# Performance work log

Hardware: AMD Instinct MI355X
Metric: run time of the kernel (lower is better)

Reference implementation:

```python
import jax, jax.numpy as jnp
import numpy as np

N_TOKEN = 267735
CUTOFFS = [20000, 40000, 200000, 267735]
ENDS = [0] + CUTOFFS
CLUSTER_DIMS = [1024, 256, 64, 16]   # d_embed // div_val**i
CLUSTER_SIZES = [20000, 20000, 160000, 67735]
D_PROJ = 1024
T, B = 256, 4
N_CLUSTERS = 3


def setup_inputs() -> dict:
    key = jax.random.key(0)
    ks = jax.random.split(key, 16)
    inp = {}
    inp["hidden"] = jax.random.normal(ks[0], (T, B, D_PROJ), jnp.float32)
    inp["target"] = jax.random.randint(ks[1], (T, B), 0, N_TOKEN)
    for i in range(4):
        inp[f"W{i}"] = jax.random.normal(ks[2 + 3 * i], (CLUSTER_SIZES[i], CLUSTER_DIMS[i]), jnp.float32) * 0.02
        inp[f"b{i}"] = jnp.zeros((CLUSTER_SIZES[i],), jnp.float32)
        inp[f"P{i}"] = jax.random.normal(ks[3 + 3 * i], (CLUSTER_DIMS[i], D_PROJ), jnp.float32) * 0.02
    inp["cluster_weight"] = jax.random.normal(ks[14], (N_CLUSTERS, 1024), jnp.float32) * 0.02
    inp["cluster_bias"] = jnp.zeros((N_CLUSTERS,), jnp.float32)
    return inp


def _logit(x, W, b, P):
    # x: [T,B,d_proj], P: [e,d_proj], W: [n,e] -> [T,B,n]
    y = jnp.einsum('ibd,ed->ibe', x, P)
    return jnp.einsum('ibe,ne->ibn', y, W) + b


def _gather(logprob, tgt):
    # pick logprob[t, b, tgt[t,b]]
    return jnp.take_along_axis(logprob, tgt[..., None], axis=-1)[..., 0]


def reference(hidden, target, W0, b0, P0, W1, b1, P1, W2, b2, P2, W3, b3, P3,
              cluster_weight, cluster_bias):
    Ws = [W0, W1, W2, W3]
    bs = [b0, b1, b2, b3]
    Ps = [P0, P1, P2, P3]
    loss = jnp.zeros(target.shape, jnp.float32)
    head_logprob = None
    for i in range(4):
        l_idx, r_idx = ENDS[i], ENDS[i + 1]
        mask = (target >= l_idx) & (target < r_idx)
        cur_t = jnp.maximum(jnp.minimum(target, r_idx - 1) - l_idx, 0)
        if i == 0:
            Wh = jnp.concatenate([W0, cluster_weight], axis=0)
            bh = jnp.concatenate([b0, cluster_bias], axis=0)
            head_logprob = jax.nn.log_softmax(_logit(hidden, Wh, bh, P0), axis=-1)
            cur_loss = _gather(head_logprob, cur_t)
        else:
            tail_logprob = jax.nn.log_softmax(_logit(hidden, Ws[i], bs[i], Ps[i]), axis=-1)
            logprob_i = head_logprob[..., CUTOFFS[0] + i - 1, None] + tail_logprob
            cur_loss = _gather(logprob_i, cur_t)
        loss = jnp.where(mask, cur_loss, loss)
    return jnp.mean(-loss)
```

## Files before the change

### kernel.cpp

```cpp
#include <hip/hip_runtime.h>
#include <math.h>

typedef short short8 __attribute__((ext_vector_type(8)));
typedef float f32x4 __attribute__((ext_vector_type(4)));
typedef unsigned long long u64;

#define LOG2E 1.4426950408889634f

#if __has_builtin(__builtin_amdgcn_exp2f)
#define EXP2(x) __builtin_amdgcn_exp2f(x)
#else
#define EXP2(x) exp2f(x)
#endif

__device__ __forceinline__ unsigned short f2bf_rne(float f) {
    unsigned u = __float_as_uint(f);
    unsigned r = (u + 0x7fff + ((u >> 16) & 1)) >> 16;
    return (unsigned short)r;
}
__device__ __forceinline__ float bf2f(unsigned short h) {
    return __uint_as_float(((unsigned)h) << 16);
}
__device__ __forceinline__ void load_lds16(const void* g, void* l) {
    __builtin_amdgcn_global_load_lds((const __attribute__((address_space(1))) void*)g,
                                     (__attribute__((address_space(3))) void*)l,
                                     16, 0, 0);
}
template<int N>
__device__ __forceinline__ void waitvm() {
    asm volatile("s_waitcnt vmcnt(%0)" :: "n"(N) : "memory");
}
__device__ __forceinline__ u64 pack8_fp8(const float* v, float s) {
    int lo = 0, hi = 0;
    lo = __builtin_amdgcn_cvt_pk_fp8_f32(v[0] * s, v[1] * s, lo, false);
    lo = __builtin_amdgcn_cvt_pk_fp8_f32(v[2] * s, v[3] * s, lo, true);
    hi = __builtin_amdgcn_cvt_pk_fp8_f32(v[4] * s, v[5] * s, hi, false);
    hi = __builtin_amdgcn_cvt_pk_fp8_f32(v[6] * s, v[7] * s, hi, true);
    return (u64)(unsigned)lo | ((u64)(unsigned)hi << 32);
}

__global__ void cvt_h(const float* __restrict__ in, unsigned short* __restrict__ out)
{
    const int i = blockIdx.x * 256 + threadIdx.x;
    const float4 v = *(const float4*)(in + (size_t)i * 4);
    ushort4 h;
    h.x = f2bf_rne(v.x); h.y = f2bf_rne(v.y);
    h.z = f2bf_rne(v.z); h.w = f2bf_rne(v.w);
    *(ushort4*)(out + (size_t)i * 4) = h;
}

struct ProjDesc {
    const float* B;
    unsigned short* Cbf;
    unsigned char* Cf8;
    int ldc; int nreal; int N; int Kpad; int gy_begin;
};

__global__ __launch_bounds__(256) void prepproj(
    const unsigned short* __restrict__ A,
    ProjDesc p0, ProjDesc p1, ProjDesc p2, ProjDesc p3,
    const float* __restrict__ W0, const float* __restrict__ cw,
    const float* __restrict__ W1, const float* __restrict__ W2,
    const float* __restrict__ W3,
    const float* __restrict__ b0, const float* __restrict__ cb,
    const float* __restrict__ b1, const float* __restrict__ b2,
    const float* __restrict__ b3,
    unsigned char* __restrict__ Wb0, unsigned char* __restrict__ Wb1,
    unsigned char* __restrict__ Wb2, unsigned char* __restrict__ Wb3,
    float* __restrict__ bp)
{
    __shared__ char smem[34816];

    const int tid = threadIdx.x;
    const int bx = blockIdx.x;

    if (bx >= 96) {
        u64* lds = (u64*)smem;
        const int NP = 2596;
        const int nconv = gridDim.x - 96;
        for (int pn = bx - 96; pn < NP; pn += nconv) {
            __syncthreads();
            if (pn < 788) {
                const bool isW0 = (pn < 628);
                const int tile = isW0 ? (pn >> 2) : (pn - 628);
                const int c0 = isW0 ? (pn & 3) * 256 : 0;
                unsigned char* dstm = isW0 ? Wb0 : Wb1;
                const int tstride = isW0 ? 131072 : 32768;
#pragma unroll
                for (int rp = 0; rp < 8; ++rp) {
                    const int row = rp * 16 + (tid >> 4);
                    const int colf = (tid & 15) * 16;
                    const int row_g = tile * 128 + row;
                    const float* s = nullptr;
                    if (isW0) {
                        if (row_g < 20000)      s = W0 + (size_t)row_g * 1024 + c0 + colf;
                        else if (row_g < 20003) s = cw + (size_t)(row_g - 20000) * 1024 + c0 + colf;
                    } else {
                        if (row_g < 20000)      s = W1 + (size_t)row_g * 256 + colf;
                    }
                    float f[16];
                    if (s) {
#pragma unroll
                        for (int q = 0; q < 4; ++q) {
                            const float4 v = *(const float4*)(s + q * 4);
                            f[q * 4 + 0] = v.x; f[q * 4 + 1] = v.y;
                            f[q * 4 + 2] = v.z; f[q * 4 + 3] = v.w;
                        }
                    } else {
#pragma unroll
                        for (int q = 0; q < 16; ++q) f[q] = 0.f;
                    }
                    const int kg = (tid & 15) * 2;
                    lds[kg * 130 + row]       = pack8_fp8(f,     16.0f);
                    lds[(kg + 1) * 130 + row] = pack8_fp8(f + 8, 16.0f);
                }
                __syncthreads();
                u64* dst = (u64*)(dstm + (size_t)tile * tstride) + (size_t)(c0 >> 3) * 128;
#pragma unroll
                for (int i = 0; i < 16; ++i) {
                    const int lin = i * 256 + tid;
                    const int kg = lin >> 7, r = lin & 127;
                    dst[lin] = lds[kg * 130 + r];
                }
            } else if (pn < 2052) {
                const int tile = pn - 788;
#pragma unroll
                for (int rp = 0; rp < 2; ++rp) {
                    const int row = rp * 64 + (tid >> 2);
                    const int colf = (tid & 3) * 16;
                    const int row_g = tile * 128 + row;
                    const float* s = (row_g < 160000) ? W2 + (size_t)row_g * 64 + colf : nullptr;
                    float f[16];
                    if (s) {
#pragma unroll
                        for (int q = 0; q < 4; ++q) {
                            const float4 v = *(const float4*)(s + q * 4);
                            f[q * 4 + 0] = v.x; f[q * 4 + 1] = v.y;
                            f[q * 4 + 2] = v.z; f[q * 4 + 3] = v.w;
                        }
                    } else {
#pragma unroll
                        for (int q = 0; q < 16; ++q) f[q] = 0.f;
                    }
                    const int kg = (tid & 3) * 2;
                    lds[kg * 130 + row]       = pack8_fp8(f,     16.0f);
                    lds[(kg + 1) * 130 + row] = pack8_fp8(f + 8, 16.0f);
                }
                __syncthreads();
                u64* dst = (u64*)(Wb2 + (size_t)tile * 8192);
#pragma unroll
                for (int i = 0; i < 4; ++i) {
                    const int lin = i * 256 + tid;
                    const int kg = lin >> 7, r = lin & 127;
                    dst[lin] = lds[kg * 130 + r];
                }
            } else {
                const int tile = pn - 2052;
                if (tid < 128) {
                    const int row = tid;
                    const int row_g = tile * 128 + row;
                    const float* s = (row_g < 67735) ? W3 + (size_t)row_g * 16 : nullptr;
                    float f[16];
                    if (s) {
#pragma unroll
                        for (int q = 0; q < 4; ++q) {
                            const float4 v = *(const float4*)(s + q * 4);
                            f[q * 4 + 0] = v.x; f[q * 4 + 1] = v.y;
                            f[q * 4 + 2] = v.z; f[q * 4 + 3] = v.w;
                        }
                    } else {
#pragma unroll
                        for (int q = 0; q < 16; ++q) f[q] = 0.f;
                    }
                    lds[row]       = pack8_fp8(f,     16.0f);
                    lds[130 + row] = pack8_fp8(f + 8, 16.0f);
                }
                __syncthreads();
                u64* dst = (u64*)(Wb3 + (size_t)tile * 8192);
#pragma unroll
                for (int i = 0; i < 4; ++i) {
                    const int lin = i * 256 + tid;
                    const int kg = lin >> 7, r = lin & 127;
                    dst[lin] = (kg < 2) ? lds[kg * 130 + r] : 0ull;
                }
            }
        }

        const unsigned BN = 68000u;
        const unsigned stride = (gridDim.x - 96) * 256u;
        for (unsigned u = (bx - 96) * 256u + tid; u < BN; u += stride) {
            const unsigned idx0 = u * 4u;
            float e[4];
#pragma unroll
            for (int j = 0; j < 4; ++j) {
                const unsigned idx = idx0 + j;
                float v;
                if (idx < 20096u) {
                    v = (idx < 20000u) ? b0[idx] * LOG2E
                      : (idx < 20003u) ? cb[idx - 20000u] * LOG2E : -1e30f;
                } else if (idx < 40576u) {
                    const unsigned i1 = idx - 20096u;
                    v = (i1 < 20000u) ? b1[i1] * LOG2E : -1e30f;
                } else if (idx < 202368u) {
                    const unsigned i2 = idx - 40576u;
                    v = (i2 < 160000u) ? b2[i2] * LOG2E : -1e30f;
                } else {
                    const unsigned i3 = idx - 202368u;
                    v = (i3 < 67735u) ? b3[i3] * LOG2E : -1e30f;
                }
                e[j] = v;
            }
            *(float4*)(bp + idx0) = make_float4(e[0], e[1], e[2], e[3]);
        }
        return;
    }

    unsigned short* As = (unsigned short*)smem;
    unsigned short* Bs = (unsigned short*)(smem + 16384);

    const int mt = bx & 7;
    const int py = bx >> 3;
    ProjDesc p = (py >= p3.gy_begin) ? p3 : (py >= p2.gy_begin) ? p2
               : (py >= p1.gy_begin) ? p1 : p0;

    const int w = tid >> 6;
    const int l = tid & 63;
    const int m0 = mt * 128;
    const int n0 = (py - p.gy_begin) * 128;
    const int wm = (w >> 1) * 64;
    const int wn = (w & 1) * 64;
    const int lane16 = l & 15;
    const int quad = l >> 4;

    const unsigned short* aptr[4];
    int ag_base[4];
#pragma unroll
    for (int i = 0; i < 4; ++i) {
        const int g = w * 256 + i * 64 + l;
        aptr[i] = A + (size_t)(m0 + (g & 127)) * 1024 + (g >> 7) * 8;
        ag_base[i] = (w * 256 + i * 64) * 8;
    }

    const int bn = tid >> 1;
    const int bhalf = tid & 1;
    int brow = n0 + bn;
    if (brow > p.N - 1) brow = p.N - 1;
    const float* brow_ptr = p.B + (size_t)brow * 1024;

    f32x4 acc[4][4] = {};

    for (int k0 = 0; k0 < 1024; k0 += 64) {
        __syncthreads();
#pragma unroll
        for (int i = 0; i < 4; ++i)
            load_lds16(aptr[i] + k0, (void*)&As[ag_base[i]]);
#pragma unroll
        for (int j = 0; j < 8; ++j) {
            const int kq = bhalf * 8 + j;
            const float4 v = *(const float4*)(brow_ptr + k0 + kq * 4);
            const unsigned px = __builtin_amdgcn_perm(__float_as_uint(v.y), __float_as_uint(v.x), 0x07060302);
            const unsigned pyv = __builtin_amdgcn_perm(__float_as_uint(v.w), __float_as_uint(v.z), 0x07060302);
            const int gran = (kq >> 1) * 128 + bn;
            *(uint2*)&Bs[gran * 8 + (kq & 1) * 4] = make_uint2(px, pyv);
        }
        __syncthreads();

#pragma unroll
        for (int kk = 0; kk < 2; ++kk) {
            const int kgb = kk * 4 + quad;
            short8 af[4], bfr[4];
#pragma unroll
            for (int mi = 0; mi < 4; ++mi)
                af[mi] = *(const short8*)&As[(kgb * 128 + wm + mi * 16 + lane16) * 8];
#pragma unroll
            for (int ni = 0; ni < 4; ++ni)
                bfr[ni] = *(const short8*)&Bs[(kgb * 128 + wn + ni * 16 + lane16) * 8];
#pragma unroll
            for (int mi = 0; mi < 4; ++mi)
#pragma unroll
                for (int ni = 0; ni < 4; ++ni)
                    acc[mi][ni] = __builtin_amdgcn_mfma_f32_16x16x32_bf16(
                        af[mi], bfr[ni], acc[mi][ni], 0, 0, 0);
        }
    }

#pragma unroll
    for (int mi = 0; mi < 4; ++mi)
#pragma unroll
        for (int ni = 0; ni < 4; ++ni) {
            const int n = n0 + wn + ni * 16 + lane16;
            if (n < p.ldc) {
#pragma unroll
                for (int r = 0; r < 4; ++r) {
                    const int m = m0 + wm + mi * 16 + quad * 4 + r;
                    const float v = (n < p.nreal) ? acc[mi][ni][r] : 0.f;
                    p.Cbf[(size_t)m * p.ldc + n] = f2bf_rne(v);
                }
            }
        }

    float* bounce = (float*)smem;
    u64* Yout = (u64*)p.Cf8 + (size_t)mt * 16 * p.Kpad;
    for (int c = 0; c < 2; ++c) {
        const int colbase = n0 + c * 64;
        if (colbase >= p.Kpad) break;
        __syncthreads();
        if ((w & 1) == c) {
#pragma unroll
            for (int mi = 0; mi < 4; ++mi)
#pragma unroll
                for (int ni = 0; ni < 4; ++ni) {
                    const int ncol = ni * 16 + lane16;
                    const bool real = (colbase + ncol) < p.nreal;
#pragma unroll
                    for (int r = 0; r < 4; ++r) {
                        const int m = wm + mi * 16 + quad * 4 + r;
                        bounce[m * 66 + ncol] = real ? acc[mi][ni][r] : 0.f;
                    }
                }
        }
        __syncthreads();
#pragma unroll
        for (int i = 0; i < 4; ++i) {
            const int g = i * 256 + tid;
            const int kgl = g >> 7;
            const int m = g & 127;
            float v[8];
#pragma unroll
            for (int j = 0; j < 8; ++j) v[j] = bounce[m * 66 + kgl * 8 + j];
            Yout[((colbase >> 3) + kgl) * 128 + m] = pack8_fp8(v, 4.0f);
        }
    }
}

struct ExpDesc {
    const unsigned char* A;
    const unsigned char* W;
    const float* bias;
    float* part;
    int Kpad; int ksl; int kmask; int gy_begin; int slab;
};

__global__ __launch_bounds__(512) void exp_gemm(ExpDesc d0, ExpDesc d1, ExpDesc d2, ExpDesc d3)
{
    __shared__ u64 As[3][2048];
    __shared__ u64 Bs[3][1024];
    __shared__ float biasLds[3][128];

    const int p = blockIdx.x;
    const int gy = blockIdx.y;

    ExpDesc d = (gy >= d3.gy_begin) ? d3 : (gy >= d2.gy_begin) ? d2
              : (gy >= d1.gy_begin) ? d1 : d0;

    const int tid = threadIdx.x;
    const int w = tid >> 6;
    const int l = tid & 63;
    const int wmt = w >> 2;
    const int wq = w & 3;
    const int wm = (wq >> 1) * 64;
    const int wn = (wq & 1) * 64;
    const int lane16 = l & 15;
    const int quad = l >> 4;

    const int tiles_begin = (gy - d.gy_begin) * d.slab;
    const int T = d.slab << d.ksl;
    const int kmask = d.kmask;
    const int ksl = d.ksl;
    const bool haveA = (kmask != 0);

    const size_t tstride = (size_t)128 * d.Kpad;
    const unsigned char* Abase0 = d.A + (size_t)p * tstride;
    const unsigned char* Abase1 = d.A + (size_t)(p + 4) * tstride;
    const unsigned char* Bbase = d.W + (size_t)tiles_begin * tstride;
    const float* biasBase = d.bias + (size_t)tiles_begin * 128;

    const int so = tid * 16;
    const int bu = (w * 4 + l) * 16;

    if (haveA) {
        load_lds16(Abase0 + so, (char*)As[0] + so);
        load_lds16(Abase1 + so, (char*)As[0] + 8192 + so);
        load_lds16(Bbase + so, (char*)Bs[0] + so);
        if (l < 4) load_lds16(biasBase + (bu >> 2), (char*)biasLds + bu);
        load_lds16(Abase0 + 8192 + so, (char*)As[1] + so);
        load_lds16(Abase1 + 8192 + so, (char*)As[1] + 8192 + so);
        load_lds16(Bbase + 8192 + so, (char*)Bs[1] + so);
        if (l < 4) load_lds16(biasBase + (bu >> 2), (char*)biasLds + 512 + bu);
    } else {
        load_lds16(Abase0 + so, (char*)As[0] + so);
        load_lds16(Abase1 + so, (char*)As[0] + 8192 + so);
        load_lds16(Bbase + so, (char*)Bs[0] + so);
        if (l < 4) load_lds16(biasBase + (bu >> 2), (char*)biasLds + bu);
        load_lds16(Bbase + tstride + so, (char*)Bs[1] + so);
        if (l < 4) load_lds16(biasBase + 128 + (bu >> 2), (char*)biasLds + 512 + bu);
    }

    f32x4 acc[4][4] = {};
    float rowsum[4][4] = {};
    const float c1 = LOG2E / 64.0f;

    int slot = 0;
    int ns = 2;
    for (int it = 0; it < T; ++it) {
        if (it + 1 < T) { if (haveA) waitvm<4>(); else waitvm<2>(); }
        else            { waitvm<0>(); }
        __builtin_amdgcn_s_barrier();
        __builtin_amdgcn_sched_barrier(0);

        if (it + 2 < T) {
            const int nit = it + 2;
            const int kc = nit & kmask;
            const int tile = nit >> ksl;
            if (haveA) {
                load_lds16(Abase0 + kc * 8192 + so, (char*)As[ns] + so);
                load_lds16(Abase1 + kc * 8192 + so, (char*)As[ns] + 8192 + so);
            }
            load_lds16(Bbase + (size_t)tile * tstride + kc * 8192 + so, (char*)Bs[ns] + so);
            if (l < 4)
                load_lds16(biasBase + (size_t)tile * 128 + (bu >> 2),
                           (char*)biasLds + ns * 512 + bu);
        }

        const u64* Ar = (haveA ? As[slot] : As[0]) + wmt * 1024;
        const u64* Br = Bs[slot];
#pragma unroll
        for (int ks = 0; ks < 2; ++ks) {
            u64 af[4], bfr[4];
#pragma unroll
            for (int mi = 0; mi < 4; ++mi)
                af[mi] = Ar[(ks * 4 + quad) * 128 + wm + mi * 16 + lane16];
#pragma unroll
            for (int ni = 0; ni < 4; ++ni)
                bfr[ni] = Br[(ks * 4 + quad) * 128 + wn + ni * 16 + lane16];
#pragma unroll
            for (int mi = 0; mi < 4; ++mi)
#pragma unroll
                for (int ni = 0; ni < 4; ++ni)
                    acc[mi][ni] = __builtin_amdgcn_mfma_f32_16x16x32_fp8_fp8(
                        (long)af[mi], (long)bfr[ni], acc[mi][ni], 0, 0, 0);
        }

        if ((it & kmask) == kmask) {
            float biasc[4];
#pragma unroll
            for (int ni = 0; ni < 4; ++ni)
                biasc[ni] = biasLds[slot][wn + ni * 16 + lane16];
#pragma unroll
            for (int mi = 0; mi < 4; ++mi)
#pragma unroll
                for (int r = 0; r < 4; ++r) {
                    float s = EXP2(fmaf(acc[mi][0][r], c1, biasc[0]))
                            + EXP2(fmaf(acc[mi][1][r], c1, biasc[1]))
                            + EXP2(fmaf(acc[mi][2][r], c1, biasc[2]))
                            + EXP2(fmaf(acc[mi][3][r], c1, biasc[3]));
                    rowsum[mi][r] += s;
                }
#pragma unroll
            for (int mi = 0; mi < 4; ++mi)
#pragma unroll
                for (int ni = 0; ni < 4; ++ni)
                    acc[mi][ni] = (f32x4){0.f, 0.f, 0.f, 0.f};
        }

        slot = (slot == 2) ? 0 : slot + 1;
        ns   = (ns   == 2) ? 0 : ns   + 1;
    }

#pragma unroll
    for (int off = 1; off < 16; off <<= 1)
#pragma unroll
        for (int mi = 0; mi < 4; ++mi)
#pragma unroll
            for (int r = 0; r < 4; ++r)
                rowsum[mi][r] += __shfl_xor(rowsum[mi][r], off, 64);

    __syncthreads();
    float* buf = (float*)As;
    if (lane16 == 0) {
#pragma unroll
        for (int mi = 0; mi < 4; ++mi)
#pragma unroll
            for (int r = 0; r < 4; ++r)
                buf[(wmt * 128 + wm + mi * 16 + quad * 4 + r) * 2 + (wn >> 6)] = rowsum[mi][r];
    }
    __syncthreads();
    if (tid < 256) {
        const int row = tid & 127;
        const int mtreal = p + (tid >> 7) * 4;
        d.part[(size_t)(gy - d.gy_begin) * 1024 + mtreal * 128 + row] =
            buf[tid * 2 + 0] + buf[tid * 2 + 1];
    }
}

__global__ void redext(const float* __restrict__ p0, const float* __restrict__ p1,
                       const float* __restrict__ p2, const float* __restrict__ p3,
                       float* __restrict__ S,
                       const unsigned short* __restrict__ Y0, const unsigned short* __restrict__ Y1,
                       const unsigned short* __restrict__ Y2, const unsigned short* __restrict__ Y3,
                       const int* __restrict__ target,
                       const float* __restrict__ W0, const float* __restrict__ b0,
                       const float* __restrict__ W1, const float* __restrict__ b1,
                       const float* __restrict__ W2, const float* __restrict__ b2,
                       const float* __restrict__ W3, const float* __restrict__ b3,
                       const float* __restrict__ cw, const float* __restrict__ cb,
                       float* __restrict__ headlogit, float* __restrict__ taillogit)
{
    if (blockIdx.x < 16) {
        const int idx = blockIdx.x * 256 + threadIdx.x;
        const int c = idx >> 10, m = idx & 1023;
        const float* p = (c == 0) ? p0 : (c == 1) ? p1 : (c == 2) ? p2 : p3;
        const int G = (c == 0) ? 157 : (c == 1) ? 40 : (c == 2) ? 79 : 34;
        float s = 0.f;
        for (int y = 0; y < G; ++y) s += p[(size_t)y * 1024 + m];
        S[idx] = s;
        return;
    }
    const int token = (blockIdx.x - 16) * 4 + (threadIdx.x >> 6);
    const int lane = threadIdx.x & 63;
    const int tgt = target[token];
    const int ci = (tgt < 20000) ? 0 : (tgt < 40000) ? 1 : (tgt < 200000) ? 2 : 3;

    {
        const int h = (ci == 0) ? tgt : (20000 + ci - 1);
        const float* row;
        float bb;
        if (h < 20000) { row = W0 + (size_t)h * 1024; bb = b0[h]; }
        else           { row = cw + (size_t)(h - 20000) * 1024; bb = cb[h - 20000]; }
        const unsigned short* y = Y0 + (size_t)token * 1024;
        float s = 0.f;
        for (int k = lane; k < 1024; k += 64) s += bf2f(y[k]) * row[k];
#pragma unroll
        for (int off = 1; off < 64; off <<= 1) s += __shfl_xor(s, off, 64);
        if (lane == 0) headlogit[token] = s + bb;
    }

    float tl = 0.f;
    if (ci > 0) {
        const unsigned short* Y; const float* W; const float* b; int K, ldy, lidx;
        if (ci == 1)      { Y = Y1; W = W1; b = b1; K = 256; ldy = 256; lidx = 20000; }
        else if (ci == 2) { Y = Y2; W = W2; b = b2; K = 64;  ldy = 64;  lidx = 40000; }
        else              { Y = Y3; W = W3; b = b3; K = 16;  ldy = 64;  lidx = 200000; }
        const int r = tgt - lidx;
        const unsigned short* y = Y + (size_t)token * ldy;
        const float* row = W + (size_t)r * K;
        float s = 0.f;
        for (int k = lane; k < K; k += 64) s += bf2f(y[k]) * row[k];
#pragma unroll
        for (int off = 1; off < 64; off <<= 1) s += __shfl_xor(s, off, 64);
        tl = s + b[r];
    }
    if (lane == 0) taillogit[token] = tl;
}

__global__ void finalize_kernel(const float* __restrict__ S,
                                const int* __restrict__ target,
                                const float* __restrict__ headlogit,
                                const float* __restrict__ taillogit,
                                float* __restrict__ out)
{
    __shared__ float red[256];
    const int tid = threadIdx.x;
    float acc = 0.f;
    for (int token = tid; token < 1024; token += 256) {
        const int tgt = target[token];
        const int ci = (tgt < 20000) ? 0 : (tgt < 40000) ? 1 : (tgt < 200000) ? 2 : 3;
        float lp = headlogit[token] - logf(S[token]);
        if (ci > 0)
            lp += taillogit[token] - logf(S[ci * 1024 + token]);
        acc -= lp;
    }
    red[tid] = acc;
    __syncthreads();
    for (int s = 128; s > 0; s >>= 1) {
        if (tid < s) red[tid] += red[tid + s];
        __syncthreads();
    }
    if (tid == 0) out[0] = red[0] * (1.0f / 1024.0f);
}

extern "C" void kernel_launch(void* const* d_in, const int* in_sizes, int n_in,
                              void* d_out, int out_size, void* d_ws, size_t ws_size,
                              hipStream_t stream)
{
    const float* hidden = (const float*)d_in[0];
    const int*   target = (const int*)d_in[1];
    const float* W0 = (const float*)d_in[2];  const float* b0 = (const float*)d_in[3];  const float* P0 = (const float*)d_in[4];
    const float* W1 = (const float*)d_in[5];  const float* b1 = (const float*)d_in[6];  const float* P1 = (const float*)d_in[7];
    const float* W2 = (const float*)d_in[8];  const float* b2 = (const float*)d_in[9];  const float* P2 = (const float*)d_in[10];
    const float* W3 = (const float*)d_in[11]; const float* b3 = (const float*)d_in[12]; const float* P3 = (const float*)d_in[13];
    const float* cw = (const float*)d_in[14]; const float* cb = (const float*)d_in[15];
    float* out = (float*)d_out;

    unsigned char* ws = (unsigned char*)d_ws;
    unsigned short* h_bf = (unsigned short*)ws;
    unsigned short* Y0bf = (unsigned short*)(ws + 2097152);
    unsigned short* Y1bf = (unsigned short*)(ws + 4194304);
    unsigned short* Y2bf = (unsigned short*)(ws + 4718592);
    unsigned short* Y3bf = (unsigned short*)(ws + 4849664);
    unsigned char* Y0f8 = ws + 4980736;
    unsigned char* Y1f8 = ws + 6029312;
    unsigned char* Y2f8 = ws + 6291456;
    unsigned char* Y3f8 = ws + 6356992;
    unsigned char* Wb0 = ws + 6422528;
    unsigned char* Wb1 = ws + 27000832;
    unsigned char* Wb2 = ws + 32243712;
    unsigned char* Wb3 = ws + 42598400;
    float* bp = (float*)(ws + 47054848);

    float* part0 = (float*)ws;
    float* part1 = part0 + (size_t)157 * 1024;
    float* part2 = part1 + (size_t)40 * 1024;
    float* part3 = part2 + (size_t)79 * 1024;
    float* S = part3 + (size_t)34 * 1024;
    float* headlogit = S + 4096;
    float* taillogit = headlogit + 1024;

    cvt_h<<<1024, 256, 0, stream>>>(hidden, h_bf);

    ProjDesc pr0 = { P0, Y0bf, Y0f8, 1024, 1024, 1024, 1024, 0 };
    ProjDesc pr1 = { P1, Y1bf, Y1f8, 256,  256,  256,  256,  8 };
    ProjDesc pr2 = { P2, Y2bf, Y2f8, 64,   64,   64,   64,   10 };
    ProjDesc pr3 = { P3, Y3bf, Y3f8, 64,   16,   16,   64,   11 };
    prepproj<<<2048, 256, 0, stream>>>(h_bf, pr0, pr1, pr2, pr3,
                                       W0, cw, W1, W2, W3,
                                       b0, cb, b1, b2, b3,
                                       Wb0, Wb1, Wb2, Wb3, bp);

    ExpDesc d0 = { Y0f8, Wb0, bp,          part0, 1024, 4, 15, 0,   1 };
    ExpDesc d1 = { Y1f8, Wb1, bp + 20096,  part1, 256,  2, 3,  157, 4 };
    ExpDesc d2 = { Y2f8, Wb2, bp + 40576,  part2, 64,   0, 0,  197, 16 };
    ExpDesc d3 = { Y3f8, Wb3, bp + 202368, part3, 64,   0, 0,  276, 16 };
    exp_gemm<<<dim3(4, 310), 512, 0, stream>>>(d0, d1, d2, d3);

    redext<<<272, 256, 0, stream>>>(part0, part1, part2, part3, S,
                                    Y0bf, Y1bf, Y2bf, Y3bf, target,
                                    W0, b0, W1, b1, W2, b2, W3, b3,
                                    cw, cb, headlogit, taillogit);

    finalize_kernel<<<1, 256, 0, stream>>>(S, target, headlogit, taillogit, out);
}
```

Before: 353.6 us.

## Double M-tiles per exp_gemm block to reuse W tiles across 1024 threads

Each exp_gemm block now covers four 128-row tiles of activations instead of two, running 1024 threads and half as many blocks along x. Each loaded W/bias tile is reused by twice as many rows, halving global weight traffic. In exchange, LDS per block grows, occupancy may drop, and only half the lanes issue B loads.

Result: slower. 383.0 us (+8.3%).

```diff
diff --git a/kernel.cpp b/kernel.cpp
--- a/kernel.cpp
+++ b/kernel.cpp
@@ -341,9 +341,9 @@
     int Kpad; int ksl; int kmask; int gy_begin; int slab;
 };
 
-__global__ __launch_bounds__(512) void exp_gemm(ExpDesc d0, ExpDesc d1, ExpDesc d2, ExpDesc d3)
+__global__ __launch_bounds__(1024) void exp_gemm(ExpDesc d0, ExpDesc d1, ExpDesc d2, ExpDesc d3)
 {
-    __shared__ u64 As[3][2048];
+    __shared__ u64 As[3][4096];
     __shared__ u64 Bs[3][1024];
     __shared__ float biasLds[3][128];
 
@@ -370,30 +370,36 @@
     const bool haveA = (kmask != 0);
 
     const size_t tstride = (size_t)128 * d.Kpad;
-    const unsigned char* Abase0 = d.A + (size_t)p * tstride;
-    const unsigned char* Abase1 = d.A + (size_t)(p + 4) * tstride;
+    const unsigned char* Abase0 = d.A + (size_t)(p * 4 + 0) * tstride;
+    const unsigned char* Abase1 = d.A + (size_t)(p * 4 + 1) * tstride;
+    const unsigned char* Abase2 = d.A + (size_t)(p * 4 + 2) * tstride;
+    const unsigned char* Abase3 = d.A + (size_t)(p * 4 + 3) * tstride;
     const unsigned char* Bbase = d.W + (size_t)tiles_begin * tstride;
     const float* biasBase = d.bias + (size_t)tiles_begin * 128;
 
     const int so = tid * 16;
-    const int bu = (w * 4 + l) * 16;
-
-    if (haveA) {
-        load_lds16(Abase0 + so, (char*)As[0] + so);
-        load_lds16(Abase1 + so, (char*)As[0] + 8192 + so);
-        load_lds16(Bbase + so, (char*)Bs[0] + so);
-        if (l < 4) load_lds16(biasBase + (bu >> 2), (char*)biasLds + bu);
-        load_lds16(Abase0 + 8192 + so, (char*)As[1] + so);
-        load_lds16(Abase1 + 8192 + so, (char*)As[1] + 8192 + so);
-        load_lds16(Bbase + 8192 + so, (char*)Bs[1] + so);
-        if (l < 4) load_lds16(biasBase + (bu >> 2), (char*)biasLds + 512 + bu);
-    } else {
-        load_lds16(Abase0 + so, (char*)As[0] + so);
-        load_lds16(Abase1 + so, (char*)As[0] + 8192 + so);
-        load_lds16(Bbase + so, (char*)Bs[0] + so);
-        if (l < 4) load_lds16(biasBase + (bu >> 2), (char*)biasLds + bu);
-        load_lds16(Bbase + tstride + so, (char*)Bs[1] + so);
-        if (l < 4) load_lds16(biasBase + 128 + (bu >> 2), (char*)biasLds + 512 + bu);
+    const unsigned char* Asrc01 = (tid < 512) ? Abase0 + so : Abase1 + (so - 8192);
+    const unsigned char* Asrc23 = (tid < 512) ? Abase2 + so : Abase3 + (so - 8192);
+    const int bo = w * 512 + l * 16;
+    const int go = w * 32 + l * 16;
+
+#pragma unroll
+    for (int pit = 0; pit < 2; ++pit) {
+        const int kc = pit & kmask;
+        const int tile = pit >> ksl;
+        if (haveA) {
+            load_lds16(Asrc01 + kc * 8192, (char*)As[pit] + so);
+            load_lds16(Asrc23 + kc * 8192, (char*)As[pit] + 16384 + so);
+        } else if (pit == 0) {
+            load_lds16(Asrc01, (char*)As[0] + so);
+            load_lds16(Asrc23, (char*)As[0] + 16384 + so);
+        }
+        if (l < 32)
+            load_lds16(Bbase + (size_t)tile * tstride + kc * 8192 + bo,
+                       (char*)Bs[pit] + bo);
+        if (l < 2)
+            load_lds16(biasBase + (size_t)tile * 128 + (go >> 2),
+                       (char*)biasLds + pit * 512 + go);
     }
 
     f32x4 acc[4][4] = {};
@@ -413,13 +419,15 @@
             const int kc = nit & kmask;
             const int tile = nit >> ksl;
             if (haveA) {
-                load_lds16(Abase0 + kc * 8192 + so, (char*)As[ns] + so);
-                load_lds16(Abase1 + kc * 8192 + so, (char*)As[ns] + 8192 + so);
+                load_lds16(Asrc01 + kc * 8192, (char*)As[ns] + so);
+                load_lds16(Asrc23 + kc * 8192, (char*)As[ns] + 16384 + so);
             }
-            load_lds16(Bbase + (size_t)tile * tstride + kc * 8192 + so, (char*)Bs[ns] + so);
-            if (l < 4)
-                load_lds16(biasBase + (size_t)tile * 128 + (bu >> 2),
-                           (char*)biasLds + ns * 512 + bu);
+            if (l < 32)
+                load_lds16(Bbase + (size_t)tile * tstride + kc * 8192 + bo,
+                           (char*)Bs[ns] + bo);
+            if (l < 2)
+                load_lds16(biasBase + (size_t)tile * 128 + (go >> 2),
+                           (char*)biasLds + ns * 512 + go);
         }
 
         const u64* Ar = (haveA ? As[slot] : As[0]) + wmt * 1024;
@@ -485,9 +493,9 @@
                 buf[(wmt * 128 + wm + mi * 16 + quad * 4 + r) * 2 + (wn >> 6)] = rowsum[mi][r];
     }
     __syncthreads();
-    if (tid < 256) {
+    if (tid < 512) {
         const int row = tid & 127;
-        const int mtreal = p + (tid >> 7) * 4;
+        const int mtreal = p * 4 + (tid >> 7);
         d.part[(size_t)(gy - d.gy_begin) * 1024 + mtreal * 128 + row] =
             buf[tid * 2 + 0] + buf[tid * 2 + 1];
     }
@@ -631,7 +639,7 @@
     ExpDesc d1 = { Y1f8, Wb1, bp + 20096,  part1, 256,  2, 3,  157, 4 };
     ExpDesc d2 = { Y2f8, Wb2, bp + 40576,  part2, 64,   0, 0,  197, 16 };
     ExpDesc d3 = { Y3f8, Wb3, bp + 202368, part3, 64,   0, 0,  276, 16 };
-    exp_gemm<<<dim3(4, 310), 512, 0, stream>>>(d0, d1, d2, d3);
+    exp_gemm<<<dim3(2, 310), 1024, 0, stream>>>(d0, d1, d2, d3);
 
     redext<<<272, 256, 0, stream>>>(part0, part1, part2, part3, S,
                                     Y0bf, Y1bf, Y2bf, Y3bf, target,
```
